# Kernel tuning notes

Hardware: AMD Instinct MI355X
Metric: run time of the kernel (lower is better)

The kernel has to match this reference:

```python
import jax, jax.numpy as jnp
import numpy as np

DIM = 768
NH = 12
HID = int(DIM * 1.5)  # 1152
B_, T_, W_ = 8, 8, 14
HW = 14 * 14
N = HW + 1
BT = B_ * T_


def _ln(x, g, b, eps=1e-5):
    m = jnp.mean(x, axis=-1, keepdims=True)
    v = jnp.var(x, axis=-1, keepdims=True)
    return (x - m) / jnp.sqrt(v + eps) * g + b


def _attn(x, wqkv, wproj, bproj, nh):
    # manual q@k^T -> softmax -> @v, as in the torch module (no qkv bias)
    b, n, c = x.shape
    hd = c // nh
    scale = hd ** -0.5
    qkv = (x @ wqkv.T).reshape(b, n, 3, nh, hd).transpose(2, 0, 3, 1, 4)
    q, k, v = qkv[0], qkv[1], qkv[2]
    a = jax.nn.softmax(jnp.einsum('bhnd,bhmd->bhnm', q, k) * scale, axis=-1)
    o = jnp.einsum('bhnm,bhmd->bhnd', a, v).transpose(0, 2, 1, 3).reshape(b, n, c)
    return o @ wproj.T + bproj


def setup_inputs() -> dict:
    key = jax.random.key(0)
    ks = jax.random.split(key, 16)
    s = 0.02
    d = {
        'x': jax.random.normal(ks[0], (BT, N, DIM), jnp.float32),
        'ln1_g': jnp.ones((DIM,), jnp.float32),
        'ln1_b': jnp.zeros((DIM,), jnp.float32),
        'qkv_w': jax.random.normal(ks[1], (3 * DIM, DIM), jnp.float32) * s,
        'proj_w': jax.random.normal(ks[2], (DIM, DIM), jnp.float32) * s,
        'proj_b': jnp.zeros((DIM,), jnp.float32),
        'tln_g': jnp.ones((DIM,), jnp.float32),
        'tln_b': jnp.zeros((DIM,), jnp.float32),
        'tqkv_w': jax.random.normal(ks[3], (3 * DIM, DIM), jnp.float32) * s,
        'tproj_w': jax.random.normal(ks[4], (DIM, DIM), jnp.float32) * s,
        'tproj_b': jnp.zeros((DIM,), jnp.float32),
        # module zero-inits temporal_fc; use small random so the branch is exercised
        'tfc_w': jax.random.normal(ks[5], (DIM, DIM), jnp.float32) * s,
        'tfc_b': jnp.zeros((DIM,), jnp.float32),
        'ln2_g': jnp.ones((DIM,), jnp.float32),
        'ln2_b': jnp.zeros((DIM,), jnp.float32),
        'fc1_w': jax.random.normal(ks[6], (HID, DIM), jnp.float32) * s,
        'fc1_b': jnp.zeros((HID,), jnp.float32),
        'fc2_w': jax.random.normal(ks[7], (DIM, HID), jnp.float32) * s,
        'fc2_b': jnp.zeros((DIM,), jnp.float32),
        'B': B_, 'T': T_, 'W': W_,
    }
    return d


def reference(x, ln1_g, ln1_b, qkv_w, proj_w, proj_b,
              tln_g, tln_b, tqkv_w, tproj_w, tproj_b, tfc_w, tfc_b,
              ln2_g, ln2_b, fc1_w, fc1_b, fc2_w, fc2_b, B, T, W):
    bt, n, c = x.shape
    hw = n - 1  # spatial tokens (cls excluded)
    # temporal branch: (b t) hw m -> (b hw) t m
    xt = x[:, 1:, :].reshape(B, T, hw, c).transpose(0, 2, 1, 3).reshape(B * hw, T, c)
    xt = _attn(_ln(xt, tln_g, tln_b), tqkv_w, tproj_w, tproj_b, NH)
    xt = xt.reshape(B, hw, T, c).transpose(0, 2, 1, 3).reshape(bt, hw, c)
    xt = xt @ tfc_w.T + tfc_b
    x = x.at[:, 1:, :].add(xt)  # in-place += in torch
    # spatial attention + residual
    x = x + _attn(_ln(x, ln1_g, ln1_b), qkv_w, proj_w, proj_b, NH)
    # MLP + residual (exact GELU, matching nn.GELU default)
    h = jax.nn.gelu(_ln(x, ln2_g, ln2_b) @ fc1_w.T + fc1_b, approximate=False)
    x = x + (h @ fc2_w.T + fc2_b)
    return x
```

## Files before the change

### kernel.cpp

```cpp
#include <hip/hip_runtime.h>
#include <hip/hip_bf16.h>


#define DIM   768
#define NH    12
#define HD    64
#define HID   1152
#define B_    8
#define T_    8
#define HW_   196
#define NTOK  197
#define BT_   64
#define MROWS (BT_ * NTOK)
#define TROWS (B_ * HW_ * T_)

typedef __bf16 bf16x8 __attribute__((ext_vector_type(8)));
typedef float  f32x4  __attribute__((ext_vector_type(4)));

__device__ inline float bf2f(ushort u) { return __uint_as_float(((unsigned)u) << 16); }
__device__ inline ushort f2bf(float f) {
    unsigned u = __float_as_uint(f);
    unsigned r = (u + 0x7fffu + ((u >> 16) & 1u)) >> 16;
    return (ushort)r;
}

__device__ inline float wred_sum(float v) {
    #pragma unroll
    for (int m = 32; m; m >>= 1) v += __shfl_xor(v, m);
    return v;
}

__device__ __forceinline__ void gload_lds16(const void* g, void* l) {
    __builtin_amdgcn_global_load_lds(
        (const __attribute__((address_space(1))) unsigned int*)g,
        (__attribute__((address_space(3))) unsigned int*)l, 16, 0, 0);
}

__device__ __forceinline__ int xcd_lin(int gid, int nwg) {
    int q = nwg >> 3, r = nwg & 7;
    int xcd = gid & 7, idx = gid >> 3;
    return (xcd < r ? xcd * (q + 1) : r * (q + 1) + (xcd - r) * q) + idx;
}

__global__ __launch_bounds__(256) void cast_all(
    const float* s0, ushort* d0, int c0, const float* s1, ushort* d1, int c1,
    const float* s2, ushort* d2, int c2, const float* s3, ushort* d3, int c3,
    const float* s4, ushort* d4, int c4, const float* s5, ushort* d5, int c5,
    const float* s6, ushort* d6, int c6)
{
    int i = blockIdx.x * 256 + threadIdx.x;
    const float* s; ushort* d; int base;
    if      (i < c0) { s = s0; d = d0; base = 0;  }
    else if (i < c1) { s = s1; d = d1; base = c0; }
    else if (i < c2) { s = s2; d = d2; base = c1; }
    else if (i < c3) { s = s3; d = d3; base = c2; }
    else if (i < c4) { s = s4; d = d4; base = c3; }
    else if (i < c5) { s = s5; d = d5; base = c4; }
    else if (i < c6) { s = s6; d = d6; base = c5; }
    else return;
    int k = i - base;
    float4 a = *(const float4*)(s + (size_t)k * 8);
    float4 b = *(const float4*)(s + (size_t)k * 8 + 4);
    ushort o[8] = {f2bf(a.x), f2bf(a.y), f2bf(a.z), f2bf(a.w),
                   f2bf(b.x), f2bf(b.y), f2bf(b.z), f2bf(b.w)};
    *(uint4*)(d + (size_t)k * 8) = *(const uint4*)o;
}

__global__ __launch_bounds__(256) void init_cls(const float* __restrict__ x, float* __restrict__ out)
{
    int i = blockIdx.x * 256 + threadIdx.x;
    int r = i / 192, c = (i % 192) * 4;
    size_t off = ((size_t)r * NTOK) * DIM + c;
    *(float4*)(out + off) = *(const float4*)(x + off);
}

enum { EPI_STORE = 0, EPI_BIAS_STORE = 1, EPI_BIAS_GELU = 2, EPI_BIAS_ADD = 3, EPI_BIAS_INIT_TFC = 4 };

template <int EPI, int KK>
__global__ __launch_bounds__(256) void gemm_bt(
    const ushort* __restrict__ Ag, const ushort* __restrict__ Wg,
    const float* __restrict__ bias, ushort* __restrict__ Cg,
    const float* __restrict__ xsrc, float* __restrict__ xf,
    int M, int N, int nm, int nn, int grp)
{
    __shared__ ushort As[2][128 * 64];
    __shared__ ushort Bs[2][128 * 64];

    const int tid  = threadIdx.x;
    const int lane = tid & 63, wid = tid >> 6;

    int lin = xcd_lin(blockIdx.x, nm * nn);
    int per = grp * nn;
    int g2 = lin / per, rem = lin % per;
    int bm = g2 * grp;
    int gm = nm - bm; if (gm > grp) gm = grp;
    const int m0 = (bm + rem % gm) * 128;
    const int n0 = (rem / gm) * 128;

    const int wm = (wid >> 1) * 64, wn = (wid & 1) * 64;
    const int fr = lane & 15, fq = lane >> 4;

    const int srow   = wid * 8 + (lane >> 3);
    const int scolsw = 8 * ((lane & 7) ^ (lane >> 3));
    const ushort* aSrc[4]; const ushort* bSrc[4];
    #pragma unroll
    for (int j = 0; j < 4; ++j) {
        int ra = m0 + j * 32 + srow; if (ra >= M) ra = M - 1;
        aSrc[j] = Ag + (size_t)ra * KK + scolsw;
        bSrc[j] = Wg + (size_t)(n0 + j * 32 + srow) * KK + scolsw;
    }

    f32x4 acc[4][4] = {};

    auto STAGE = [&](int buf, int k0) {
        #pragma unroll
        for (int j = 0; j < 4; ++j) {
            gload_lds16(aSrc[j] + k0, &As[buf][(j * 32 + wid * 8) * 64]);
            gload_lds16(bSrc[j] + k0, &Bs[buf][(j * 32 + wid * 8) * 64]);
        }
    };

    auto COMPUTE = [&](int buf) {
        #pragma unroll
        for (int ks = 0; ks < 2; ++ks) {
            bf16x8 af[4], bfr[4];
            #pragma unroll
            for (int i = 0; i < 4; ++i)
                af[i] = *(const bf16x8*)&As[buf][(wm + i * 16 + fr) * 64 +
                                                ((ks * 32 + fq * 8) ^ ((fr & 7) * 8))];
            #pragma unroll
            for (int j = 0; j < 4; ++j)
                bfr[j] = *(const bf16x8*)&Bs[buf][(wn + j * 16 + fr) * 64 +
                                                 ((ks * 32 + fq * 8) ^ ((fr & 7) * 8))];
            #pragma unroll
            for (int i = 0; i < 4; ++i)
                #pragma unroll
                for (int j = 0; j < 4; ++j)
                    acc[i][j] = __builtin_amdgcn_mfma_f32_16x16x32_bf16(af[i], bfr[j], acc[i][j], 0, 0, 0);
        }
    };

    constexpr int NT = KK / 64;
    STAGE(0, 0);
    STAGE(1, 64);
    #pragma unroll
    for (int t = 0; t < NT; ++t) {
        if (t + 2 < NT) asm volatile("s_waitcnt vmcnt(8)" ::: "memory");
        else if (t + 1 < NT) asm volatile("s_waitcnt vmcnt(8)" ::: "memory");
        else asm volatile("s_waitcnt vmcnt(0)" ::: "memory");
        __builtin_amdgcn_s_barrier();
        __builtin_amdgcn_sched_barrier(0);
        COMPUTE(t & 1);
        __builtin_amdgcn_sched_barrier(0);
        __builtin_amdgcn_s_barrier();
        __builtin_amdgcn_sched_barrier(0);
        if (t + 2 < NT) STAGE(t & 1, (t + 2) * 64);
    }

    #pragma unroll
    for (int i = 0; i < 4; ++i) {
        #pragma unroll
        for (int e = 0; e < 4; ++e) {
            int row = m0 + wm + i * 16 + fq * 4 + e;
            if (row >= M) continue;
            #pragma unroll
            for (int j = 0; j < 4; ++j) {
                int col = n0 + wn + j * 16 + fr;
                float v = acc[i][j][e];
                if constexpr (EPI != EPI_STORE) v += bias[col];
                if constexpr (EPI == EPI_BIAS_GELU) v = 0.5f * v * (1.0f + erff(v * 0.70710678118654752f));
                if constexpr (EPI == EPI_STORE || EPI == EPI_BIAS_STORE || EPI == EPI_BIAS_GELU) {
                    Cg[(size_t)row * N + col] = f2bf(v);
                } else if constexpr (EPI == EPI_BIAS_ADD) {
                    xf[(size_t)row * DIM + col] += v;
                } else {
                    int t2 = row & 7, pp = (row >> 3) % HW_, bb = row / (HW_ * T_);
                    size_t dst = ((size_t)(bb * T_ + t2) * NTOK + 1 + pp) * DIM + col;
                    xf[dst] = xsrc[dst] + v;
                }
            }
        }
    }
}

__global__ __launch_bounds__(256) void ln_f32(
    const float* __restrict__ src, const float* __restrict__ g,
    const float* __restrict__ b, ushort* __restrict__ dst, int rows)
{
    int widx = threadIdx.x >> 6, lane = threadIdx.x & 63;
    int r = blockIdx.x * 4 + widx;
    if (r >= rows) return;
    const float* row = src + (size_t)r * DIM;
    float v[12], sum = 0.f, sq = 0.f;
    #pragma unroll
    for (int c = 0; c < 3; ++c) {
        float4 t = *(const float4*)(row + c * 256 + lane * 4);
        v[c*4+0] = t.x; v[c*4+1] = t.y; v[c*4+2] = t.z; v[c*4+3] = t.w;
        sum += t.x + t.y + t.z + t.w;
        sq  += t.x*t.x + t.y*t.y + t.z*t.z + t.w*t.w;
    }
    sum = wred_sum(sum); sq = wred_sum(sq);
    float mean = sum * (1.f / DIM);
    float var  = sq * (1.f / DIM) - mean * mean;
    float rstd = rsqrtf(var + 1e-5f);
    #pragma unroll
    for (int c = 0; c < 3; ++c) {
        int idx = c * 256 + lane * 4;
        float4 gg = *(const float4*)(g + idx);
        float4 bb = *(const float4*)(b + idx);
        ushort4 o;
        o.x = f2bf((v[c*4+0] - mean) * rstd * gg.x + bb.x);
        o.y = f2bf((v[c*4+1] - mean) * rstd * gg.y + bb.y);
        o.z = f2bf((v[c*4+2] - mean) * rstd * gg.z + bb.z);
        o.w = f2bf((v[c*4+3] - mean) * rstd * gg.w + bb.w);
        *(ushort4*)(dst + (size_t)r * DIM + idx) = o;
    }
}

__global__ __launch_bounds__(256) void ln_gather(
    const float* __restrict__ x, const float* __restrict__ g,
    const float* __restrict__ b, ushort* __restrict__ dst, int rows)
{
    int widx = threadIdx.x >> 6, lane = threadIdx.x & 63;
    int r = blockIdx.x * 4 + widx;
    if (r >= rows) return;
    int t = r & 7, pp = (r >> 3) % HW_, bb = r / (HW_ * T_);
    const float* row = x + ((size_t)(bb * T_ + t) * NTOK + 1 + pp) * DIM;
    float v[12], sum = 0.f, sq = 0.f;
    #pragma unroll
    for (int c = 0; c < 3; ++c) {
        float4 t4 = *(const float4*)(row + c * 256 + lane * 4);
        v[c*4+0] = t4.x; v[c*4+1] = t4.y; v[c*4+2] = t4.z; v[c*4+3] = t4.w;
        sum += t4.x + t4.y + t4.z + t4.w;
        sq  += t4.x*t4.x + t4.y*t4.y + t4.z*t4.z + t4.w*t4.w;
    }
    sum = wred_sum(sum); sq = wred_sum(sq);
    float mean = sum * (1.f / DIM);
    float var  = sq * (1.f / DIM) - mean * mean;
    float rstd = rsqrtf(var + 1e-5f);
    #pragma unroll
    for (int c = 0; c < 3; ++c) {
        int idx = c * 256 + lane * 4;
        float4 gg = *(const float4*)(g + idx);
        float4 bb2 = *(const float4*)(b + idx);
        ushort4 o;
        o.x = f2bf((v[c*4+0] - mean) * rstd * gg.x + bb2.x);
        o.y = f2bf((v[c*4+1] - mean) * rstd * gg.y + bb2.y);
        o.z = f2bf((v[c*4+2] - mean) * rstd * gg.z + bb2.z);
        o.w = f2bf((v[c*4+3] - mean) * rstd * gg.w + bb2.w);
        *(ushort4*)(dst + (size_t)r * DIM + idx) = o;
    }
}

__global__ __launch_bounds__(256) void attn_temporal(
    const ushort* __restrict__ qkv, ushort* __restrict__ O)
{
    int widx = threadIdx.x >> 6, lane = threadIdx.x & 63;
    int w = blockIdx.x * 4 + widx;
    int s = w / NH, h = w % NH;
    int qi = lane >> 3, kj = lane & 7;

    const ushort* qrow = qkv + (size_t)(s * 8 + qi) * (3 * DIM) + h * HD;
    const ushort* krow = qkv + (size_t)(s * 8 + kj) * (3 * DIM) + DIM + h * HD;
    float d = 0.f;
    #pragma unroll
    for (int c = 0; c < 8; ++c) {
        uint4 qa = *(const uint4*)(qrow + c * 8);
        uint4 ka = *(const uint4*)(krow + c * 8);
        const ushort* qs = (const ushort*)&qa;
        const ushort* ks = (const ushort*)&ka;
        #pragma unroll
        for (int e = 0; e < 8; ++e) d += bf2f(qs[e]) * bf2f(ks[e]);
    }
    float sc = d * 0.125f;
    float mx = sc;
    #pragma unroll
    for (int m = 4; m; m >>= 1) mx = fmaxf(mx, __shfl_xor(mx, m));
    float p = expf(sc - mx);
    float sum = p;
    #pragma unroll
    for (int m = 4; m; m >>= 1) sum += __shfl_xor(sum, m);
    p /= sum;

    float o[8] = {};
    int base = lane & ~7;
    #pragma unroll
    for (int t = 0; t < 8; ++t) {
        float pt = __shfl(p, base + t);
        const ushort* vrow = qkv + (size_t)(s * 8 + t) * (3 * DIM) + 2 * DIM + h * HD + kj * 8;
        uint4 va = *(const uint4*)vrow;
        const ushort* vs = (const ushort*)&va;
        #pragma unroll
        for (int e = 0; e < 8; ++e) o[e] += pt * bf2f(vs[e]);
    }
    ushort out[8];
    #pragma unroll
    for (int e = 0; e < 8; ++e) out[e] = f2bf(o[e]);
    *(uint4*)(O + (size_t)(s * 8 + qi) * DIM + h * HD + kj * 8) = *(const uint4*)out;
}

#define KS_STRIDE 72
#define VT_STRIDE 208
#define P_STRIDE  208
#define KS_OFF    0
#define VT_OFF    (197 * KS_STRIDE)
#define P_OFF     (VT_OFF + 64 * VT_STRIDE)
#define LDS_TOT   (P_OFF + 4 * 16 * P_STRIDE)

__global__ __launch_bounds__(256, 2) void attn_spatial_mfma(
    const ushort* __restrict__ qkv, ushort* __restrict__ O)
{
    __shared__ ushort lds[LDS_TOT];
    const int tid = threadIdx.x, lane = tid & 63, wid = tid >> 6;
    const int fr = lane & 15, fq = lane >> 4;
    int lin = xcd_lin(blockIdx.x, BT_ * NH);
    const int s = lin / NH, h = lin % NH;
    const size_t base = (size_t)s * NTOK * (3 * DIM);
    const ushort* Qg = qkv + base + h * HD;
    const ushort* Kg = qkv + base + DIM + h * HD;
    const ushort* Vg = qkv + base + 2 * DIM + h * HD;

    for (int chunk = tid; chunk < NTOK * 8; chunk += 256) {
        int r = chunk >> 3, c = (chunk & 7) * 8;
        uint4 v = *(const uint4*)(Kg + (size_t)r * (3 * DIM) + c);
        *(uint4*)&lds[KS_OFF + r * KS_STRIDE + c] = v;
    }
    for (int chunk = tid; chunk < 208 * 8; chunk += 256) {
        int k = chunk >> 3, c = (chunk & 7) * 8;
        uint4 v = {0u, 0u, 0u, 0u};
        if (k < NTOK) v = *(const uint4*)(Vg + (size_t)k * (3 * DIM) + c);
        const ushort* e = (const ushort*)&v;
        #pragma unroll
        for (int j = 0; j < 8; ++j) lds[VT_OFF + (c + j) * VT_STRIDE + k] = e[j];
    }
    __syncthreads();

    ushort* P = &lds[P_OFF + wid * 16 * P_STRIDE];

    for (int qi = wid; qi < 13; qi += 4) {
        int qrow = qi * 16 + fr; if (qrow > NTOK - 1) qrow = NTOK - 1;
        bf16x8 qf0 = *(const bf16x8*)(Qg + (size_t)qrow * (3 * DIM) + fq * 8);
        bf16x8 qf1 = *(const bf16x8*)(Qg + (size_t)qrow * (3 * DIM) + 32 + fq * 8);

        f32x4 sacc[13];
        #pragma unroll
        for (int t = 0; t < 13; ++t) {
            bf16x8 kf0 = *(const bf16x8*)&lds[KS_OFF + (t * 16 + fr) * KS_STRIDE + fq * 8];
            bf16x8 kf1 = *(const bf16x8*)&lds[KS_OFF + (t * 16 + fr) * KS_STRIDE + 32 + fq * 8];
            f32x4 z = {0.f, 0.f, 0.f, 0.f};
            z = __builtin_amdgcn_mfma_f32_16x16x32_bf16(kf0, qf0, z, 0, 0, 0);
            sacc[t] = __builtin_amdgcn_mfma_f32_16x16x32_bf16(kf1, qf1, z, 0, 0, 0);
        }

        float m = -1e30f;
        #pragma unroll
        for (int t = 0; t < 13; ++t)
            #pragma unroll
            for (int e = 0; e < 4; ++e) {
                int k = t * 16 + fq * 4 + e;
                float v = (k < NTOK) ? sacc[t][e] * 0.125f : -1e30f;
                sacc[t][e] = v;
                m = fmaxf(m, v);
            }
        m = fmaxf(m, __shfl_xor(m, 16));
        m = fmaxf(m, __shfl_xor(m, 32));
        float sum = 0.f;
        #pragma unroll
        for (int t = 0; t < 13; ++t)
            #pragma unroll
            for (int e = 0; e < 4; ++e) {
                float p = expf(sacc[t][e] - m);
                sacc[t][e] = p;
                sum += p;
            }
        sum += __shfl_xor(sum, 16);
        sum += __shfl_xor(sum, 32);
        float rd = 1.f / sum;

        #pragma unroll
        for (int t = 0; t < 13; ++t) {
            ushort2 w0 = { f2bf(sacc[t][0] * rd), f2bf(sacc[t][1] * rd) };
            ushort2 w1 = { f2bf(sacc[t][2] * rd), f2bf(sacc[t][3] * rd) };
            *(ushort2*)&P[fr * P_STRIDE + t * 16 + fq * 4]     = w0;
            *(ushort2*)&P[fr * P_STRIDE + t * 16 + fq * 4 + 2] = w1;
        }

        f32x4 oacc[4] = {};
        #pragma unroll
        for (int st = 0; st < 6; ++st) {
            bf16x8 pf = *(const bf16x8*)&P[fr * P_STRIDE + st * 32 + fq * 8];
            #pragma unroll
            for (int dt = 0; dt < 4; ++dt) {
                bf16x8 vf = *(const bf16x8*)&lds[VT_OFF + (dt * 16 + fr) * VT_STRIDE + st * 32 + fq * 8];
                oacc[dt] = __builtin_amdgcn_mfma_f32_16x16x32_bf16(pf, vf, oacc[dt], 0, 0, 0);
            }
        }
        {
            bf16x8 zz = {};
            bf16x8 pf = zz;
            if (fq < 2) pf = *(const bf16x8*)&P[fr * P_STRIDE + 192 + fq * 8];
            #pragma unroll
            for (int dt = 0; dt < 4; ++dt) {
                bf16x8 vf = zz;
                if (fq < 2) vf = *(const bf16x8*)&lds[VT_OFF + (dt * 16 + fr) * VT_STRIDE + 192 + fq * 8];
                oacc[dt] = __builtin_amdgcn_mfma_f32_16x16x32_bf16(pf, vf, oacc[dt], 0, 0, 0);
            }
        }

        #pragma unroll
        for (int dt = 0; dt < 4; ++dt)
            #pragma unroll
            for (int e = 0; e < 4; ++e) {
                int q = qi * 16 + fq * 4 + e;
                if (q < NTOK)
                    O[(size_t)(s * NTOK + q) * DIM + h * HD + dt * 16 + fr] = f2bf(oacc[dt][e]);
            }
    }
}

extern "C" void kernel_launch(void* const* d_in, const int* in_sizes, int n_in,
                              void* d_out, int out_size, void* d_ws, size_t ws_size,
                              hipStream_t stream)
{
    const float* x      = (const float*)d_in[0];
    const float* ln1_g  = (const float*)d_in[1];
    const float* ln1_b  = (const float*)d_in[2];
    const float* qkv_w  = (const float*)d_in[3];
    const float* proj_w = (const float*)d_in[4];
    const float* proj_b = (const float*)d_in[5];
    const float* tln_g  = (const float*)d_in[6];
    const float* tln_b  = (const float*)d_in[7];
    const float* tqkv_w = (const float*)d_in[8];
    const float* tproj_w= (const float*)d_in[9];
    const float* tproj_b= (const float*)d_in[10];
    const float* tfc_w  = (const float*)d_in[11];
    const float* tfc_b  = (const float*)d_in[12];
    const float* ln2_g  = (const float*)d_in[13];
    const float* ln2_b  = (const float*)d_in[14];
    const float* fc1_w  = (const float*)d_in[15];
    const float* fc1_b  = (const float*)d_in[16];
    const float* fc2_w  = (const float*)d_in[17];
    const float* fc2_b  = (const float*)d_in[18];

    float* out = (float*)d_out;

    char* p = (char*)d_ws;
    ushort* w_qkv  = (ushort*)p; p += (size_t)(3*DIM*DIM) * 2;
    ushort* w_proj = (ushort*)p; p += (size_t)(DIM*DIM) * 2;
    ushort* w_tqkv = (ushort*)p; p += (size_t)(3*DIM*DIM) * 2;
    ushort* w_tproj= (ushort*)p; p += (size_t)(DIM*DIM) * 2;
    ushort* w_tfc  = (ushort*)p; p += (size_t)(DIM*DIM) * 2;
    ushort* w_fc1  = (ushort*)p; p += (size_t)(HID*DIM) * 2;
    ushort* w_fc2  = (ushort*)p; p += (size_t)(HID*DIM) * 2;
    ushort* bufA   = (ushort*)p; p += (size_t)MROWS * DIM * 2;
    ushort* bufC   = (ushort*)p; p += (size_t)MROWS * DIM * 2;
    ushort* bufB   = (ushort*)p;

    {
        const int DD8 = DIM * DIM / 8;
        int c0 = 3 * DD8;
        int c1 = c0 + DD8;
        int c2 = c1 + 3 * DD8;
        int c3 = c2 + DD8;
        int c4 = c3 + DD8;
        int c5 = c4 + HID * DIM / 8;
        int c6 = c5 + HID * DIM / 8;
        cast_all<<<dim3((c6 + 255) / 256), dim3(256), 0, stream>>>(
            qkv_w, w_qkv, c0, proj_w, w_proj, c1, tqkv_w, w_tqkv, c2,
            tproj_w, w_tproj, c3, tfc_w, w_tfc, c4, fc1_w, w_fc1, c5,
            fc2_w, w_fc2, c6);
    }

    init_cls<<<dim3(48), dim3(256), 0, stream>>>(x, out);

    auto grid = [](int M, int N) { return dim3(((M + 127) / 128) * (N / 128)); };
    #define GEMM(EPI, KV, A, W, BIAS, C, XS, XF, M, N, GRP) \
        gemm_bt<EPI, KV><<<grid(M, N), dim3(256), 0, stream>>>( \
            A, W, BIAS, C, XS, XF, M, N, (M + 127) / 128, (N) / 128, GRP)

    ln_gather<<<dim3(TROWS / 4), dim3(256), 0, stream>>>(x, tln_g, tln_b, bufA, TROWS);
    GEMM(EPI_STORE, DIM, bufA, w_tqkv, nullptr, bufB, nullptr, nullptr, TROWS, 3 * DIM, 2);
    attn_temporal<<<dim3(TROWS * NH / 8 / 4), dim3(256), 0, stream>>>(bufB, bufC);
    GEMM(EPI_BIAS_STORE, DIM, bufC, w_tproj, tproj_b, bufA, nullptr, nullptr, TROWS, DIM, 8);
    GEMM(EPI_BIAS_INIT_TFC, DIM, bufA, w_tfc, tfc_b, nullptr, x, out, TROWS, DIM, 8);

    ln_f32<<<dim3((MROWS + 3) / 4), dim3(256), 0, stream>>>(out, ln1_g, ln1_b, bufA, MROWS);
    GEMM(EPI_STORE, DIM, bufA, w_qkv, nullptr, bufB, nullptr, nullptr, MROWS, 3 * DIM, 2);
    attn_spatial_mfma<<<dim3(BT_ * NH), dim3(256), 0, stream>>>(bufB, bufC);
    GEMM(EPI_BIAS_ADD, DIM, bufC, w_proj, proj_b, nullptr, nullptr, out, MROWS, DIM, 8);

    ln_f32<<<dim3((MROWS + 3) / 4), dim3(256), 0, stream>>>(out, ln2_g, ln2_b, bufA, MROWS);
    GEMM(EPI_BIAS_GELU, DIM, bufA, w_fc1, fc1_b, bufB, nullptr, nullptr, MROWS, HID, 8);
    GEMM(EPI_BIAS_ADD, HID, bufB, w_fc2, fc2_b, nullptr, nullptr, out, MROWS, DIM, 4);
    #undef GEMM
}
```

Before: 424.4 us.

## Add 256x256-tile 512-thread GEMM for the two QKV projections

```diff
diff --git a/kernel.cpp b/kernel.cpp
--- a/kernel.cpp
+++ b/kernel.cpp
@@ -41,6 +41,8 @@
     int xcd = gid & 7, idx = gid >> 3;
     return (xcd < r ? xcd * (q + 1) : r * (q + 1) + (xcd - r) * q) + idx;
 }
+
+#define MFMA16(a, b, c) __builtin_amdgcn_mfma_f32_16x16x32_bf16(a, b, c, 0, 0, 0)
 
 __global__ __launch_bounds__(256) void cast_all(
     const float* s0, ushort* d0, int c0, const float* s1, ushort* d1, int c1,
@@ -74,6 +76,151 @@
     *(float4*)(out + off) = *(const float4*)(x + off);
 }
 
+template <int KK>
+__global__ __launch_bounds__(512, 1) void gemm256(
+    const ushort* __restrict__ Ag, const ushort* __restrict__ Wg,
+    ushort* __restrict__ Cg, int M, int N, int nm, int nn, int grp)
+{
+    __shared__ ushort As[2][256 * 64];
+    __shared__ ushort Bs[2][256 * 64];
+
+    const int tid  = threadIdx.x;
+    const int lane = tid & 63, wid = tid >> 6;
+    const int wr = wid >> 2, wc = wid & 3;
+    const int fr = lane & 15, fq = lane >> 4;
+
+    int lin = xcd_lin(blockIdx.x, nm * nn);
+    int per = grp * nn;
+    int g2 = lin / per, rem = lin % per;
+    int bm = g2 * grp;
+    int gm = nm - bm; if (gm > grp) gm = grp;
+    const int m0 = (bm + rem % gm) * 256;
+    const int n0 = (rem / gm) * 256;
+
+    const int srow = wid * 8 + (lane >> 3);
+    const int scol = 8 * ((lane & 7) ^ (lane >> 3));
+    const ushort* aP[4]; const ushort* bP[4];
+    #pragma unroll
+    for (int j = 0; j < 4; ++j) {
+        int ra = m0 + j * 64 + srow; if (ra >= M) ra = M - 1;
+        aP[j] = Ag + (size_t)ra * KK + scol;
+        bP[j] = Wg + (size_t)(n0 + j * 64 + srow) * KK + scol;
+    }
+    const int ldso = (wid * 8) * 64;
+
+    f32x4 acc[8][4] = {};
+    bf16x8 af[4][2], b0[2][2], b1[2][2];
+
+    const int sw0 = (fq * 8) ^ ((fr & 7) * 8);
+    const int sw1 = (32 + fq * 8) ^ ((fr & 7) * 8);
+
+    #pragma unroll
+    for (int j = 0; j < 4; ++j) gload_lds16(aP[j], &As[0][j * 4096 + ldso]);
+    #pragma unroll
+    for (int j = 0; j < 4; ++j) gload_lds16(bP[j], &Bs[0][j * 4096 + ldso]);
+
+    constexpr int NT = KK / 64;
+    #pragma unroll
+    for (int t = 0; t < NT; ++t) {
+        const int rb = t & 1, wb = rb ^ 1;
+        const bool st = (t + 1 < NT);
+        const int kw = (t + 1) * 64;
+
+        asm volatile("s_waitcnt vmcnt(0)" ::: "memory");
+        __builtin_amdgcn_s_barrier();
+        __builtin_amdgcn_sched_barrier(0);
+
+        #pragma unroll
+        for (int mf = 0; mf < 4; ++mf) {
+            af[mf][0] = *(const bf16x8*)&As[rb][(wr * 128 + mf * 16 + fr) * 64 + sw0];
+            af[mf][1] = *(const bf16x8*)&As[rb][(wr * 128 + mf * 16 + fr) * 64 + sw1];
+        }
+        #pragma unroll
+        for (int nf = 0; nf < 2; ++nf) {
+            b0[nf][0] = *(const bf16x8*)&Bs[rb][(wc * 64 + nf * 16 + fr) * 64 + sw0];
+            b0[nf][1] = *(const bf16x8*)&Bs[rb][(wc * 64 + nf * 16 + fr) * 64 + sw1];
+        }
+        if (st) {
+            #pragma unroll
+            for (int j = 0; j < 4; ++j) gload_lds16(aP[j] + kw, &As[wb][j * 4096 + ldso]);
+        }
+        asm volatile("s_waitcnt lgkmcnt(0)" ::: "memory");
+        __builtin_amdgcn_sched_barrier(0);
+        __builtin_amdgcn_s_setprio(1);
+        #pragma unroll
+        for (int mf = 0; mf < 4; ++mf)
+            #pragma unroll
+            for (int nf = 0; nf < 2; ++nf) {
+                acc[mf][nf] = MFMA16(af[mf][0], b0[nf][0], acc[mf][nf]);
+                acc[mf][nf] = MFMA16(af[mf][1], b0[nf][1], acc[mf][nf]);
+            }
+        __builtin_amdgcn_s_setprio(0);
+        __builtin_amdgcn_sched_barrier(0);
+
+        #pragma unroll
+        for (int nf = 0; nf < 2; ++nf) {
+            b1[nf][0] = *(const bf16x8*)&Bs[rb][(wc * 64 + (nf + 2) * 16 + fr) * 64 + sw0];
+            b1[nf][1] = *(const bf16x8*)&Bs[rb][(wc * 64 + (nf + 2) * 16 + fr) * 64 + sw1];
+        }
+        if (st) {
+            #pragma unroll
+            for (int j = 0; j < 4; ++j) gload_lds16(bP[j] + kw, &Bs[wb][j * 4096 + ldso]);
+        }
+        asm volatile("s_waitcnt lgkmcnt(0)" ::: "memory");
+        __builtin_amdgcn_sched_barrier(0);
+        __builtin_amdgcn_s_setprio(1);
+        #pragma unroll
+        for (int mf = 0; mf < 4; ++mf)
+            #pragma unroll
+            for (int nf = 0; nf < 2; ++nf) {
+                acc[mf][nf + 2] = MFMA16(af[mf][0], b1[nf][0], acc[mf][nf + 2]);
+                acc[mf][nf + 2] = MFMA16(af[mf][1], b1[nf][1], acc[mf][nf + 2]);
+            }
+        __builtin_amdgcn_s_setprio(0);
+        __builtin_amdgcn_sched_barrier(0);
+
+        #pragma unroll
+        for (int mf = 0; mf < 4; ++mf) {
+            af[mf][0] = *(const bf16x8*)&As[rb][(wr * 128 + 64 + mf * 16 + fr) * 64 + sw0];
+            af[mf][1] = *(const bf16x8*)&As[rb][(wr * 128 + 64 + mf * 16 + fr) * 64 + sw1];
+        }
+        asm volatile("s_waitcnt lgkmcnt(0)" ::: "memory");
+        __builtin_amdgcn_sched_barrier(0);
+        __builtin_amdgcn_s_setprio(1);
+        #pragma unroll
+        for (int mf = 0; mf < 4; ++mf)
+            #pragma unroll
+            for (int nf = 0; nf < 2; ++nf) {
+                acc[mf + 4][nf] = MFMA16(af[mf][0], b0[nf][0], acc[mf + 4][nf]);
+                acc[mf + 4][nf] = MFMA16(af[mf][1], b0[nf][1], acc[mf + 4][nf]);
+            }
+        __builtin_amdgcn_s_setprio(0);
+        __builtin_amdgcn_sched_barrier(0);
+
+        __builtin_amdgcn_s_setprio(1);
+        #pragma unroll
+        for (int mf = 0; mf < 4; ++mf)
+            #pragma unroll
+            for (int nf = 0; nf < 2; ++nf) {
+                acc[mf + 4][nf + 2] = MFMA16(af[mf][0], b1[nf][0], acc[mf + 4][nf + 2]);
+                acc[mf + 4][nf + 2] = MFMA16(af[mf][1], b1[nf][1], acc[mf + 4][nf + 2]);
+            }
+        __builtin_amdgcn_s_setprio(0);
+        __builtin_amdgcn_sched_barrier(0);
+    }
+
+    #pragma unroll
+    for (int mf = 0; mf < 8; ++mf)
+        #pragma unroll
+        for (int e = 0; e < 4; ++e) {
+            int row = m0 + wr * 128 + mf * 16 + fq * 4 + e;
+            if (row >= M) continue;
+            #pragma unroll
+            for (int nf = 0; nf < 4; ++nf)
+                Cg[(size_t)row * N + n0 + wc * 64 + nf * 16 + fr] = f2bf(acc[mf][nf][e]);
+        }
+}
+
 enum { EPI_STORE = 0, EPI_BIAS_STORE = 1, EPI_BIAS_GELU = 2, EPI_BIAS_ADD = 3, EPI_BIAS_INIT_TFC = 4 };
 
 template <int EPI, int KK>
@@ -136,7 +283,7 @@
             for (int i = 0; i < 4; ++i)
                 #pragma unroll
                 for (int j = 0; j < 4; ++j)
-                    acc[i][j] = __builtin_amdgcn_mfma_f32_16x16x32_bf16(af[i], bfr[j], acc[i][j], 0, 0, 0);
+                    acc[i][j] = MFMA16(af[i], bfr[j], acc[i][j]);
         }
     };
 
@@ -145,8 +292,7 @@
     STAGE(1, 64);
     #pragma unroll
     for (int t = 0; t < NT; ++t) {
-        if (t + 2 < NT) asm volatile("s_waitcnt vmcnt(8)" ::: "memory");
-        else if (t + 1 < NT) asm volatile("s_waitcnt vmcnt(8)" ::: "memory");
+        if (t + 1 < NT) asm volatile("s_waitcnt vmcnt(8)" ::: "memory");
         else asm volatile("s_waitcnt vmcnt(0)" ::: "memory");
         __builtin_amdgcn_s_barrier();
         __builtin_amdgcn_sched_barrier(0);
@@ -348,8 +494,8 @@
             bf16x8 kf0 = *(const bf16x8*)&lds[KS_OFF + (t * 16 + fr) * KS_STRIDE + fq * 8];
             bf16x8 kf1 = *(const bf16x8*)&lds[KS_OFF + (t * 16 + fr) * KS_STRIDE + 32 + fq * 8];
             f32x4 z = {0.f, 0.f, 0.f, 0.f};
-            z = __builtin_amdgcn_mfma_f32_16x16x32_bf16(kf0, qf0, z, 0, 0, 0);
-            sacc[t] = __builtin_amdgcn_mfma_f32_16x16x32_bf16(kf1, qf1, z, 0, 0, 0);
+            z = MFMA16(kf0, qf0, z);
+            sacc[t] = MFMA16(kf1, qf1, z);
         }
 
         float m = -1e30f;
@@ -392,7 +538,7 @@
             #pragma unroll
             for (int dt = 0; dt < 4; ++dt) {
                 bf16x8 vf = *(const bf16x8*)&lds[VT_OFF + (dt * 16 + fr) * VT_STRIDE + st * 32 + fq * 8];
-                oacc[dt] = __builtin_amdgcn_mfma_f32_16x16x32_bf16(pf, vf, oacc[dt], 0, 0, 0);
+                oacc[dt] = MFMA16(pf, vf, oacc[dt]);
             }
         }
         {
@@ -403,7 +549,7 @@
             for (int dt = 0; dt < 4; ++dt) {
                 bf16x8 vf = zz;
                 if (fq < 2) vf = *(const bf16x8*)&lds[VT_OFF + (dt * 16 + fr) * VT_STRIDE + 192 + fq * 8];
-                oacc[dt] = __builtin_amdgcn_mfma_f32_16x16x32_bf16(pf, vf, oacc[dt], 0, 0, 0);
+                oacc[dt] = MFMA16(pf, vf, oacc[dt]);
             }
         }
 
@@ -473,19 +619,21 @@
 
     init_cls<<<dim3(48), dim3(256), 0, stream>>>(x, out);
 
-    auto grid = [](int M, int N) { return dim3(((M + 127) / 128) * (N / 128)); };
     #define GEMM(EPI, KV, A, W, BIAS, C, XS, XF, M, N, GRP) \
-        gemm_bt<EPI, KV><<<grid(M, N), dim3(256), 0, stream>>>( \
-            A, W, BIAS, C, XS, XF, M, N, (M + 127) / 128, (N) / 128, GRP)
+        gemm_bt<EPI, KV><<<dim3((((M) + 127) / 128) * ((N) / 128)), dim3(256), 0, stream>>>( \
+            A, W, BIAS, C, XS, XF, M, N, ((M) + 127) / 128, (N) / 128, GRP)
+    #define GEMM256(KV, A, W, C, M, N, GRP) \
+        gemm256<KV><<<dim3((((M) + 255) / 256) * ((N) / 256)), dim3(512), 0, stream>>>( \
+            A, W, C, M, N, ((M) + 255) / 256, (N) / 256, GRP)
 
     ln_gather<<<dim3(TROWS / 4), dim3(256), 0, stream>>>(x, tln_g, tln_b, bufA, TROWS);
-    GEMM(EPI_STORE, DIM, bufA, w_tqkv, nullptr, bufB, nullptr, nullptr, TROWS, 3 * DIM, 2);
+    GEMM256(DIM, bufA, w_tqkv, bufB, TROWS, 3 * DIM, 1);
     attn_temporal<<<dim3(TROWS * NH / 8 / 4), dim3(256), 0, stream>>>(bufB, bufC);
     GEMM(EPI_BIAS_STORE, DIM, bufC, w_tproj, tproj_b, bufA, nullptr, nullptr, TROWS, DIM, 8);
     GEMM(EPI_BIAS_INIT_TFC, DIM, bufA, w_tfc, tfc_b, nullptr, x, out, TROWS, DIM, 8);
 
     ln_f32<<<dim3((MROWS + 3) / 4), dim3(256), 0, stream>>>(out, ln1_g, ln1_b, bufA, MROWS);
-    GEMM(EPI_STORE, DIM, bufA, w_qkv, nullptr, bufB, nullptr, nullptr, MROWS, 3 * DIM, 2);
+    GEMM256(DIM, bufA, w_qkv, bufB, MROWS, 3 * DIM, 1);
     attn_spatial_mfma<<<dim3(BT_ * NH), dim3(256), 0, stream>>>(bufB, bufC);
     GEMM(EPI_BIAS_ADD, DIM, bufC, w_proj, proj_b, nullptr, nullptr, out, MROWS, DIM, 8);
 
@@ -493,4 +641,5 @@
     GEMM(EPI_BIAS_GELU, DIM, bufA, w_fc1, fc1_b, bufB, nullptr, nullptr, MROWS, HID, 8);
     GEMM(EPI_BIAS_ADD, HID, bufB, w_fc2, fc2_b, nullptr, nullptr, out, MROWS, DIM, 4);
     #undef GEMM
-}
+    #undef GEMM256
+}
```

New measurement: 415.5 us. 1.02x faster.
